# Kernel tuning notes

Hardware: AMD Instinct MI355X
Metric: run time of the kernel (lower is better)

The kernel has to match this reference:

```python
import jax, jax.numpy as jnp
import numpy as np

N, E = 50000, 600000
IN_C, HID, OUT_C = 256, 128, 2
R, B, L = 7, 8, 3
ALPHA = 0.1


def _rgcn(x, src, dst, etype, comp, basis, root, bias):
    # comp: [R,B], basis: [B,d,d] -> per-relation weights W: [R,d,d]
    n, d = x.shape
    W = jnp.einsum('rb,bdf->rdf', comp, basis)
    # combined (dst, relation) segment id for per-relation mean aggregation
    seg = dst * R + etype
    msg = x[src]  # [E,d] gather
    s = jax.ops.segment_sum(msg, seg, num_segments=n * R)  # [N*R,d]
    cnt = jax.ops.segment_sum(jnp.ones((E,), x.dtype), seg, num_segments=n * R)
    agg = (s / jnp.maximum(cnt, 1.0)[:, None]).reshape(n, R, d)  # per-relation mean
    return x @ root + bias + jnp.einsum('nrd,rdf->nf', agg, W)


def setup_inputs() -> dict:
    key = jax.random.key(0)
    ks = jax.random.split(key, 10)
    sc = 0.05
    x = jax.random.normal(ks[0], (N, IN_C), dtype=jnp.float32)
    edge_index = jax.random.randint(ks[1], (2, E), 0, N)
    edge_type = jax.random.randint(ks[2], (E,), 0, R)
    # GPR temp init: alpha*(1-alpha)^k, last entry (1-alpha)^K
    temp = jnp.asarray(ALPHA * (1.0 - ALPHA) ** np.arange(L + 1), dtype=jnp.float32)
    temp = temp.at[-1].set((1.0 - ALPHA) ** L)
    lin1_w = jax.random.normal(ks[3], (IN_C, HID), jnp.float32) * sc
    lin1_b = jnp.zeros((HID,), jnp.float32)
    lin2_w = jax.random.normal(ks[4], (HID, OUT_C), jnp.float32) * sc
    lin2_b = jnp.zeros((OUT_C,), jnp.float32)
    comps = jax.random.normal(ks[5], (L, R, B), jnp.float32) * sc
    bases = jax.random.normal(ks[6], (L, B, HID, HID), jnp.float32) * sc
    roots = jax.random.normal(ks[7], (L, HID, HID), jnp.float32) * sc
    conv_biases = jnp.zeros((L, HID), jnp.float32)
    return dict(x=x, edge_index=edge_index, edge_type=edge_type, temp=temp,
                lin1_w=lin1_w, lin1_b=lin1_b, lin2_w=lin2_w, lin2_b=lin2_b,
                comps=comps, bases=bases, roots=roots, conv_biases=conv_biases)


def reference(x, edge_index, edge_type, temp, lin1_w, lin1_b, lin2_w, lin2_b,
              comps, bases, roots, conv_biases):
    src, dst = edge_index[0], edge_index[1]
    h = x @ lin1_w + lin1_b
    hidden = h * temp[0]
    cur = hidden
    for i in range(L):
        cur = _rgcn(cur, src, dst, edge_type, comps[i], bases[i], roots[i], conv_biases[i])
        if i < L - 1:
            cur = jax.nn.relu(cur)  # dropout p=0.4 is identity in eval mode
        hidden = hidden + temp[i + 1] * cur
    return hidden @ lin2_w + lin2_b
```

## Files before the change

### kernel.cpp

```cpp
#include <hip/hip_runtime.h>
#include <cstdint>


constexpr int N_NODES  = 50000;
constexpr int E_EDGES  = 600000;
constexpr int R_REL    = 7;
constexpr int HID      = 128;
constexpr int IN_C     = 256;
constexpr int L_LAYERS = 3;
constexpr int AGG_COLS = 896;
constexpr int K_CAT    = 1024;
constexpr int NR       = N_NODES * R_REL;
constexpr int SCANR_BLOCKS = (NR + 255) / 256;

#define DEVI __device__ __forceinline__

using short8  = __attribute__((ext_vector_type(8))) short;
using floatx4 = __attribute__((ext_vector_type(4))) float;

DEVI unsigned short f2bf(float f) {
  unsigned u = __float_as_uint(f);
  unsigned r = (u + 0x7FFFu + ((u >> 16) & 1u)) >> 16;
  return (unsigned short)r;
}
DEVI float bf2f(unsigned short h) { return __uint_as_float(((unsigned)h) << 16); }

__global__ __launch_bounds__(256) void cast_w1_kernel(
    const float* __restrict__ w1, unsigned short* __restrict__ w1T)
{
  int t = blockIdx.x * 256 + threadIdx.x;
  if (t >= HID * IN_C) return;
  int m = t >> 8, k = t & 255;
  w1T[m * IN_C + k] = f2bf(w1[k * HID + m]);
}

__global__ __launch_bounds__(256) void build_wcat2(
    const float* __restrict__ comps,
    const float* __restrict__ bases,
    const float* __restrict__ roots,
    unsigned short* __restrict__ wcat2T)
{
  int t = blockIdx.x * 256 + threadIdx.x;
  if (t >= L_LAYERS * 128 * K_CAT) return;
  int l   = t >> 17;
  int rem = t & 131071;
  int f   = rem >> 10;
  int k   = rem & 1023;
  float v;
  if (k < 128) {
    v = roots[((size_t)l * 128 + k) * 128 + f];
  } else {
    int r = (k - 128) >> 7, d = (k - 128) & 127;
    const float* cp = comps + ((size_t)l * R_REL + r) * 8;
    const float* bp = bases + (((size_t)l * 8) * 128 + d) * 128 + f;
    float s = 0.f;
#pragma unroll
    for (int b = 0; b < 8; ++b) s += cp[b] * bp[(size_t)b * 128 * 128];
    v = s;
  }
  wcat2T[t] = f2bf(v);
}

__global__ __launch_bounds__(256) void hist_kernel(
    const int* __restrict__ ei, const int* __restrict__ et,
    int* __restrict__ cntRel, int* __restrict__ erank)
{
  int e = blockIdx.x * 256 + threadIdx.x;
  if (e >= E_EDGES) return;
  int seg = ei[E_EDGES + e] * R_REL + et[e];
  erank[e] = atomicAdd(&cntRel[seg], 1);
}

__global__ __launch_bounds__(256) void scanA_kernel(
    const int* __restrict__ cnt, int* __restrict__ tmpOff,
    int* __restrict__ blockSums)
{
  __shared__ int s[256];
  int i = blockIdx.x * 256 + threadIdx.x;
  int v = (i < NR) ? cnt[i] : 0;
  s[threadIdx.x] = v;
  __syncthreads();
#pragma unroll
  for (int d = 1; d < 256; d <<= 1) {
    int t = (threadIdx.x >= d) ? s[threadIdx.x - d] : 0;
    __syncthreads();
    s[threadIdx.x] += t;
    __syncthreads();
  }
  if (i < NR) tmpOff[i] = s[threadIdx.x] - v;
  if (threadIdx.x == 255) blockSums[blockIdx.x] = s[255];
}

__global__ __launch_bounds__(256) void scanB_kernel(int* __restrict__ bs)
{
  __shared__ int s[256];
  __shared__ int carry;
  if (threadIdx.x == 0) carry = 0;
  __syncthreads();
  for (int base = 0; base < SCANR_BLOCKS; base += 256) {
    int cOld = carry;
    int i = base + threadIdx.x;
    int v = (i < SCANR_BLOCKS) ? bs[i] : 0;
    s[threadIdx.x] = v;
    __syncthreads();
#pragma unroll
    for (int d = 1; d < 256; d <<= 1) {
      int t = (threadIdx.x >= d) ? s[threadIdx.x - d] : 0;
      __syncthreads();
      s[threadIdx.x] += t;
      __syncthreads();
    }
    if (i < SCANR_BLOCKS) bs[i] = s[threadIdx.x] - v + cOld;
    __syncthreads();
    if (threadIdx.x == 0) carry = cOld + s[255];
    __syncthreads();
  }
}

__global__ __launch_bounds__(256) void scanC_kernel(
    const int* __restrict__ tmpOff, const int* __restrict__ blockSums,
    int* __restrict__ drs)
{
  int i = blockIdx.x * 256 + threadIdx.x;
  if (i < NR) drs[i] = tmpOff[i] + blockSums[blockIdx.x];
  if (i == 0) drs[NR] = E_EDGES;
}

__global__ __launch_bounds__(256) void place_kernel(
    const int* __restrict__ ei, const int* __restrict__ et,
    const int* __restrict__ drs, const int* __restrict__ erank,
    unsigned short* __restrict__ esrc)
{
  int e = blockIdx.x * 256 + threadIdx.x;
  if (e >= E_EDGES) return;
  int seg = ei[E_EDGES + e] * R_REL + et[e];
  int pos = drs[seg] + erank[e];
  esrc[pos] = (unsigned short)ei[e];
}

constexpr int AGG_NPF = 16;
__global__ __launch_bounds__(256) void agg_reg_kernel(
    const unsigned short* __restrict__ curA,
    const unsigned short* __restrict__ esrc,
    const int* __restrict__ drs,
    unsigned short* __restrict__ aggB)
{
  const int tid  = threadIdx.x;
  const int lane = tid & 63;
  const int dst  = blockIdx.x * 4 + (tid >> 6);
  if (dst >= N_NODES) return;
  const int segBase = dst * R_REL;

  int bnd = drs[segBase + (lane & 7)];
  const int a0    = __shfl(bnd, 0);
  const int total = __shfl(bnd, 7) - a0;

  int pk = 0;
  if (lane < total) pk = (int)esrc[a0 + lane];

  const unsigned* colp = (const unsigned*)curA + lane;
  unsigned* outp = (unsigned*)(aggB + (size_t)dst * AGG_COLS) + lane;

  int r = 0;
  int segStart = 0;
  int segEnd = __shfl(bnd, 1) - a0;
  float sx = 0.f, sy = 0.f;
  int pos = 0;

#define AGG_FLUSH()                                                        \
  while (r < R_REL && segEnd == pos) {                                     \
    int c = segEnd - segStart;                                             \
    float sc = (c > 0) ? 1.0f / (float)c : 0.f;                            \
    unsigned pck = (unsigned)f2bf(sx * sc) | ((unsigned)f2bf(sy * sc) << 16); \
    outp[r * 64] = pck;                                                    \
    sx = 0.f; sy = 0.f;                                                    \
    segStart = segEnd;                                                     \
    ++r;                                                                   \
    segEnd = (r < R_REL) ? (__shfl(bnd, r + 1) - a0) : 0x7FFFFFFF;         \
  }

  AGG_FLUSH();

  for (int base = 0; base < total; base += AGG_NPF) {
    const int cnt = min(total - base, AGG_NPF);
    unsigned v[AGG_NPF];
#pragma unroll
    for (int e = 0; e < AGG_NPF; ++e) {
      if (e < cnt) {
        int idx = base + e;
        int src = (idx < 64) ? __shfl(pk, idx) : (int)esrc[a0 + idx];
        v[e] = colp[src * 64];
      }
    }
#pragma unroll
    for (int e = 0; e < AGG_NPF; ++e) {
      if (e >= cnt) break;
      unsigned u = v[e];
      sx += __uint_as_float(u << 16);
      sy += __uint_as_float(u & 0xFFFF0000u);
      ++pos;
      AGG_FLUSH();
    }
  }
#undef AGG_FLUSH
}

__global__ __launch_bounds__(256) void gemm_lin1(
    const float* __restrict__ x,
    const unsigned short* __restrict__ BT,
    const float* __restrict__ bias,
    const float* __restrict__ temp,
    unsigned short* __restrict__ b0out)
{
  __shared__ unsigned short Atile[64][136];
  __shared__ unsigned short Btile[128][136];
  const int tid  = threadIdx.x;
  const int row0 = blockIdx.x * 64;
  const int lane = tid & 63;
  const int wid  = tid >> 6;
  const int wrow = (wid & 1) * 32;
  const int wcol = (wid >> 1) * 64;
  const int l15  = lane & 15;
  const int quad = lane >> 4;

  floatx4 acc[2][4] = {};

  for (int k0 = 0; k0 < IN_C; k0 += 128) {
#pragma unroll
    for (int it = 0; it < 4; ++it) {
      int chunk = it * 256 + tid;
      int r = chunk >> 4, cc = (chunk & 15) << 3;
      int grow = row0 + r;
      uint4 va = make_uint4(0u, 0u, 0u, 0u);
      if (grow < N_NODES) {
        const float* xp = x + (size_t)grow * IN_C + k0 + cc;
        float4 f0 = *(const float4*)xp;
        float4 f1 = *(const float4*)(xp + 4);
        va.x = (unsigned)f2bf(f0.x) | ((unsigned)f2bf(f0.y) << 16);
        va.y = (unsigned)f2bf(f0.z) | ((unsigned)f2bf(f0.w) << 16);
        va.z = (unsigned)f2bf(f1.x) | ((unsigned)f2bf(f1.y) << 16);
        va.w = (unsigned)f2bf(f1.z) | ((unsigned)f2bf(f1.w) << 16);
      }
      *(uint4*)(&Atile[r][cc]) = va;
    }
#pragma unroll
    for (int it = 0; it < 8; ++it) {
      int chunk = it * 256 + tid;
      int n = chunk >> 4, cc = (chunk & 15) << 3;
      *(uint4*)(&Btile[n][cc]) =
          *(const uint4*)(BT + (size_t)n * IN_C + k0 + cc);
    }
    __syncthreads();
#pragma unroll
    for (int ks = 0; ks < 4; ++ks) {
      int kc = ks * 32 + quad * 8;
      short8 af[2], bfr[4];
#pragma unroll
      for (int i = 0; i < 2; ++i)
        af[i] = *(const short8*)(&Atile[wrow + i * 16 + l15][kc]);
#pragma unroll
      for (int j = 0; j < 4; ++j)
        bfr[j] = *(const short8*)(&Btile[wcol + j * 16 + l15][kc]);
#pragma unroll
      for (int i = 0; i < 2; ++i)
#pragma unroll
        for (int j = 0; j < 4; ++j)
          acc[i][j] = __builtin_amdgcn_mfma_f32_16x16x32_bf16(
              af[i], bfr[j], acc[i][j], 0, 0, 0);
    }
    __syncthreads();
  }

  float t0 = temp[0];
#pragma unroll
  for (int i = 0; i < 2; ++i) {
    int lrow0 = wrow + i * 16 + quad * 4;
#pragma unroll
    for (int j = 0; j < 4; ++j) {
      int gcol = wcol + j * 16 + l15;
      float bb = bias[gcol];
#pragma unroll
      for (int r = 0; r < 4; ++r)
        Atile[lrow0 + r][gcol] = f2bf(t0 * (acc[i][j][r] + bb));
    }
  }
  __syncthreads();
#pragma unroll
  for (int it = 0; it < 4; ++it) {
    int chunk = it * 256 + tid;
    int r = chunk >> 4, cc = (chunk & 15) << 3;
    int grow = row0 + r;
    if (grow < N_NODES)
      *(uint4*)(b0out + (size_t)grow * HID + cc) = *(const uint4*)(&Atile[r][cc]);
  }
}

__global__ __launch_bounds__(256) void gemm_layer(
    const unsigned short* __restrict__ curA,
    const unsigned short* __restrict__ aggB,
    const unsigned short* __restrict__ BT,
    const float* __restrict__ bias,
    unsigned short* __restrict__ bout,
    int layer)
{
  __shared__ unsigned short Atile[64][136];
  __shared__ unsigned short Btile[128][136];
  const int tid  = threadIdx.x;
  const int row0 = blockIdx.x * 64;
  const int lane = tid & 63;
  const int wid  = tid >> 6;
  const int wrow = (wid & 1) * 32;
  const int wcol = (wid >> 1) * 64;
  const int l15  = lane & 15;
  const int quad = lane >> 4;

  floatx4 acc[2][4] = {};

  for (int p = 0; p < 8; ++p) {
#pragma unroll
    for (int it = 0; it < 8; ++it) {
      int chunk = it * 256 + tid;
      int n = chunk >> 4, cc = (chunk & 15) << 3;
      *(uint4*)(&Btile[n][cc]) =
          *(const uint4*)(BT + (size_t)n * K_CAT + p * 128 + cc);
    }
#pragma unroll
    for (int it = 0; it < 4; ++it) {
      int chunk = it * 256 + tid;
      int r = chunk >> 4, cc = (chunk & 15) << 3;
      int grow = row0 + r;
      uint4 va = make_uint4(0u, 0u, 0u, 0u);
      if (grow < N_NODES) {
        if (p == 0)
          va = *(const uint4*)(curA + (size_t)grow * HID + cc);
        else
          va = *(const uint4*)(aggB + (size_t)grow * AGG_COLS +
                               (p - 1) * 128 + cc);
      }
      *(uint4*)(&Atile[r][cc]) = va;
    }
    __syncthreads();
#pragma unroll
    for (int ks = 0; ks < 4; ++ks) {
      int kc = ks * 32 + quad * 8;
      short8 af[2], bfr[4];
#pragma unroll
      for (int i = 0; i < 2; ++i)
        af[i] = *(const short8*)(&Atile[wrow + i * 16 + l15][kc]);
#pragma unroll
      for (int j = 0; j < 4; ++j)
        bfr[j] = *(const short8*)(&Btile[wcol + j * 16 + l15][kc]);
#pragma unroll
      for (int i = 0; i < 2; ++i)
#pragma unroll
        for (int j = 0; j < 4; ++j)
          acc[i][j] = __builtin_amdgcn_mfma_f32_16x16x32_bf16(
              af[i], bfr[j], acc[i][j], 0, 0, 0);
    }
    __syncthreads();
  }

  const bool isLast = (layer == L_LAYERS - 1);
#pragma unroll
  for (int i = 0; i < 2; ++i) {
    int lrow0 = wrow + i * 16 + quad * 4;
#pragma unroll
    for (int j = 0; j < 4; ++j) {
      int gcol = wcol + j * 16 + l15;
      float bb = bias[gcol];
#pragma unroll
      for (int r = 0; r < 4; ++r) {
        float c = acc[i][j][r] + bb;
        if (!isLast) c = fmaxf(c, 0.f);
        Atile[lrow0 + r][gcol] = f2bf(c);
      }
    }
  }
  __syncthreads();
#pragma unroll
  for (int it = 0; it < 4; ++it) {
    int chunk = it * 256 + tid;
    int r = chunk >> 4, cc = (chunk & 15) << 3;
    int grow = row0 + r;
    if (grow < N_NODES)
      *(uint4*)(bout + (size_t)grow * HID + cc) = *(const uint4*)(&Atile[r][cc]);
  }
}

__global__ __launch_bounds__(256) void final_kernel(
    const unsigned short* __restrict__ b0, const unsigned short* __restrict__ b1,
    const unsigned short* __restrict__ b2v, const unsigned short* __restrict__ b3,
    const float* __restrict__ temp,
    const float* __restrict__ w2, const float* __restrict__ b2bias,
    float* __restrict__ out)
{
  int node = blockIdx.x * 4 + (threadIdx.x >> 6);
  int lane = threadIdx.x & 63;
  if (node >= N_NODES) return;
  float t1 = temp[1], t2 = temp[2], t3 = temp[3];
  size_t base = (size_t)node * 64 + lane;
  unsigned u0 = ((const unsigned*)b0)[base];
  unsigned u1 = ((const unsigned*)b1)[base];
  unsigned u2 = ((const unsigned*)b2v)[base];
  unsigned u3 = ((const unsigned*)b3)[base];
  float hx = bf2f((unsigned short)(u0 & 0xFFFF)) +
             t1 * bf2f((unsigned short)(u1 & 0xFFFF)) +
             t2 * bf2f((unsigned short)(u2 & 0xFFFF)) +
             t3 * bf2f((unsigned short)(u3 & 0xFFFF));
  float hy = bf2f((unsigned short)(u0 >> 16)) +
             t1 * bf2f((unsigned short)(u1 >> 16)) +
             t2 * bf2f((unsigned short)(u2 >> 16)) +
             t3 * bf2f((unsigned short)(u3 >> 16));
  int d0 = lane * 2, d1 = lane * 2 + 1;
  float a0 = hx * w2[d0 * 2 + 0] + hy * w2[d1 * 2 + 0];
  float a1 = hx * w2[d0 * 2 + 1] + hy * w2[d1 * 2 + 1];
#pragma unroll
  for (int off = 32; off > 0; off >>= 1) {
    a0 += __shfl_down(a0, off);
    a1 += __shfl_down(a1, off);
  }
  if (lane == 0) {
    out[node * 2 + 0] = a0 + b2bias[0];
    out[node * 2 + 1] = a1 + b2bias[1];
  }
}

extern "C" void kernel_launch(void* const* d_in, const int* in_sizes, int n_in,
                              void* d_out, int out_size, void* d_ws, size_t ws_size,
                              hipStream_t stream) {
  const float* x     = (const float*)d_in[0];
  const int*   ei    = (const int*)d_in[1];
  const int*   et    = (const int*)d_in[2];
  const float* temp  = (const float*)d_in[3];
  const float* w1    = (const float*)d_in[4];
  const float* b1    = (const float*)d_in[5];
  const float* w2    = (const float*)d_in[6];
  const float* b2    = (const float*)d_in[7];
  const float* comps = (const float*)d_in[8];
  const float* bases = (const float*)d_in[9];
  const float* roots = (const float*)d_in[10];
  const float* cbias = (const float*)d_in[11];

  char* ws = (char*)d_ws;
  size_t off = 0;
  auto take = [&](size_t bytes) {
    char* p = ws + off;
    off = (off + bytes + 255) & ~(size_t)255;
    return p;
  };
  unsigned short* wcat2T = (unsigned short*)take((size_t)L_LAYERS * 128 * K_CAT * 2);
  unsigned short* w1T    = (unsigned short*)take((size_t)HID * IN_C * 2);
  int*   cntRel  = (int*)take((size_t)NR * 4);
  int*   tmpOffR = (int*)take((size_t)NR * 4);
  int*   blockSumsR = (int*)take((size_t)SCANR_BLOCKS * 4);
  int*   drs     = (int*)take((size_t)(NR + 1) * 4);
  int*   erank   = (int*)take((size_t)E_EDGES * 4);
  unsigned short* esrc = (unsigned short*)take((size_t)E_EDGES * 2);
  unsigned short* bl[L_LAYERS + 1];
  for (int i = 0; i <= L_LAYERS; ++i)
    bl[i] = (unsigned short*)take((size_t)N_NODES * HID * 2);
  unsigned short* aggB = (unsigned short*)take((size_t)N_NODES * AGG_COLS * 2);

  hipMemsetAsync(cntRel, 0, (size_t)NR * 4, stream);

  hipLaunchKernelGGL(build_wcat2, dim3((L_LAYERS * 128 * K_CAT + 255) / 256),
                     dim3(256), 0, stream, comps, bases, roots, wcat2T);
  hipLaunchKernelGGL(cast_w1_kernel, dim3((HID * IN_C + 255) / 256), dim3(256),
                     0, stream, w1, w1T);
  hipLaunchKernelGGL(hist_kernel, dim3((E_EDGES + 255) / 256), dim3(256), 0,
                     stream, ei, et, cntRel, erank);
  hipLaunchKernelGGL(scanA_kernel, dim3(SCANR_BLOCKS), dim3(256), 0, stream,
                     cntRel, tmpOffR, blockSumsR);
  hipLaunchKernelGGL(scanB_kernel, dim3(1), dim3(256), 0, stream, blockSumsR);
  hipLaunchKernelGGL(scanC_kernel, dim3(SCANR_BLOCKS), dim3(256), 0, stream,
                     tmpOffR, blockSumsR, drs);
  hipLaunchKernelGGL(place_kernel, dim3((E_EDGES + 255) / 256), dim3(256), 0,
                     stream, ei, et, drs, erank, esrc);

  const int rowBlocks64 = (N_NODES + 63) / 64;
  hipLaunchKernelGGL(gemm_lin1, dim3(rowBlocks64), dim3(256), 0, stream,
                     x, w1T, b1, temp, bl[0]);

  for (int l = 0; l < L_LAYERS; ++l) {
    hipLaunchKernelGGL(agg_reg_kernel, dim3((N_NODES + 3) / 4), dim3(256),
                       0, stream, bl[l], esrc, drs, aggB);
    hipLaunchKernelGGL(gemm_layer, dim3(rowBlocks64), dim3(256), 0, stream,
                       bl[l], aggB, wcat2T + (size_t)l * 128 * K_CAT,
                       cbias + (size_t)l * HID, bl[l + 1], l);
  }

  hipLaunchKernelGGL(final_kernel, dim3((N_NODES + 3) / 4), dim3(256), 0, stream,
                     bl[0], bl[1], bl[2], bl[3], temp, w2, b2, (float*)d_out);
}
```

Measured before the change: 496.5 us.

## Load GEMM A fragments directly from global and widen row tile to 128

The layer GEMM now reads its A operand (current features and aggregated neighbours) straight from global memory into MFMA registers, no longer staging it in shared memory, and each block covers 128 rows instead of 64 with a 4x4 accumulator grid per wave. This halves how often the shared B tile is reloaded per row and removes A's LDS traffic, at the cost of more registers and uncoalesced 16-byte row-strided global loads. The two weight-preparation kernels are also merged into one launch to save a kernel launch.

```diff
diff --git a/kernel.cpp b/kernel.cpp
--- a/kernel.cpp
+++ b/kernel.cpp
@@ -12,6 +12,7 @@
 constexpr int K_CAT    = 1024;
 constexpr int NR       = N_NODES * R_REL;
 constexpr int SCANR_BLOCKS = (NR + 255) / 256;
+constexpr int WCAT_ELEMS = L_LAYERS * 128 * K_CAT;
 
 #define DEVI __device__ __forceinline__
 
@@ -25,40 +26,40 @@
 }
 DEVI float bf2f(unsigned short h) { return __uint_as_float(((unsigned)h) << 16); }
 
-__global__ __launch_bounds__(256) void cast_w1_kernel(
-    const float* __restrict__ w1, unsigned short* __restrict__ w1T)
-{
-  int t = blockIdx.x * 256 + threadIdx.x;
-  if (t >= HID * IN_C) return;
-  int m = t >> 8, k = t & 255;
-  w1T[m * IN_C + k] = f2bf(w1[k * HID + m]);
-}
-
-__global__ __launch_bounds__(256) void build_wcat2(
+__global__ __launch_bounds__(256) void prep_weights(
+    const float* __restrict__ w1,
     const float* __restrict__ comps,
     const float* __restrict__ bases,
     const float* __restrict__ roots,
+    unsigned short* __restrict__ w1T,
     unsigned short* __restrict__ wcat2T)
 {
   int t = blockIdx.x * 256 + threadIdx.x;
-  if (t >= L_LAYERS * 128 * K_CAT) return;
-  int l   = t >> 17;
-  int rem = t & 131071;
-  int f   = rem >> 10;
-  int k   = rem & 1023;
-  float v;
-  if (k < 128) {
-    v = roots[((size_t)l * 128 + k) * 128 + f];
+  if (t < WCAT_ELEMS) {
+    int l   = t >> 17;
+    int rem = t & 131071;
+    int f   = rem >> 10;
+    int k   = rem & 1023;
+    float v;
+    if (k < 128) {
+      v = roots[((size_t)l * 128 + k) * 128 + f];
+    } else {
+      int r = (k - 128) >> 7, d = (k - 128) & 127;
+      const float* cp = comps + ((size_t)l * R_REL + r) * 8;
+      const float* bp = bases + (((size_t)l * 8) * 128 + d) * 128 + f;
+      float s = 0.f;
+#pragma unroll
+      for (int b = 0; b < 8; ++b) s += cp[b] * bp[(size_t)b * 128 * 128];
+      v = s;
+    }
+    wcat2T[t] = f2bf(v);
   } else {
-    int r = (k - 128) >> 7, d = (k - 128) & 127;
-    const float* cp = comps + ((size_t)l * R_REL + r) * 8;
-    const float* bp = bases + (((size_t)l * 8) * 128 + d) * 128 + f;
-    float s = 0.f;
-#pragma unroll
-    for (int b = 0; b < 8; ++b) s += cp[b] * bp[(size_t)b * 128 * 128];
-    v = s;
-  }
-  wcat2T[t] = f2bf(v);
+    int u = t - WCAT_ELEMS;
+    if (u < HID * IN_C) {
+      int m = u >> 8, k = u & 255;
+      w1T[m * IN_C + k] = f2bf(w1[k * HID + m]);
+    }
+  }
 }
 
 __global__ __launch_bounds__(256) void hist_kernel(
@@ -303,18 +304,17 @@
     unsigned short* __restrict__ bout,
     int layer)
 {
-  __shared__ unsigned short Atile[64][136];
   __shared__ unsigned short Btile[128][136];
   const int tid  = threadIdx.x;
-  const int row0 = blockIdx.x * 64;
+  const int row0 = blockIdx.x * 128;
   const int lane = tid & 63;
   const int wid  = tid >> 6;
-  const int wrow = (wid & 1) * 32;
+  const int wrow = (wid & 1) * 64;
   const int wcol = (wid >> 1) * 64;
   const int l15  = lane & 15;
   const int quad = lane >> 4;
 
-  floatx4 acc[2][4] = {};
+  floatx4 acc[4][4] = {};
 
   for (int p = 0; p < 8; ++p) {
 #pragma unroll
@@ -324,34 +324,28 @@
       *(uint4*)(&Btile[n][cc]) =
           *(const uint4*)(BT + (size_t)n * K_CAT + p * 128 + cc);
     }
-#pragma unroll
-    for (int it = 0; it < 4; ++it) {
-      int chunk = it * 256 + tid;
-      int r = chunk >> 4, cc = (chunk & 15) << 3;
-      int grow = row0 + r;
-      uint4 va = make_uint4(0u, 0u, 0u, 0u);
-      if (grow < N_NODES) {
-        if (p == 0)
-          va = *(const uint4*)(curA + (size_t)grow * HID + cc);
-        else
-          va = *(const uint4*)(aggB + (size_t)grow * AGG_COLS +
-                               (p - 1) * 128 + cc);
-      }
-      *(uint4*)(&Atile[r][cc]) = va;
-    }
     __syncthreads();
 #pragma unroll
     for (int ks = 0; ks < 4; ++ks) {
       int kc = ks * 32 + quad * 8;
-      short8 af[2], bfr[4];
-#pragma unroll
-      for (int i = 0; i < 2; ++i)
-        af[i] = *(const short8*)(&Atile[wrow + i * 16 + l15][kc]);
+      short8 af[4], bfr[4];
+#pragma unroll
+      for (int i = 0; i < 4; ++i) {
+        int grow = row0 + wrow + i * 16 + l15;
+        short8 v = {};
+        if (grow < N_NODES) {
+          const unsigned short* ap = (p == 0)
+              ? curA + (size_t)grow * HID + kc
+              : aggB + (size_t)grow * AGG_COLS + (p - 1) * 128 + kc;
+          v = *(const short8*)ap;
+        }
+        af[i] = v;
+      }
 #pragma unroll
       for (int j = 0; j < 4; ++j)
         bfr[j] = *(const short8*)(&Btile[wcol + j * 16 + l15][kc]);
 #pragma unroll
-      for (int i = 0; i < 2; ++i)
+      for (int i = 0; i < 4; ++i)
 #pragma unroll
         for (int j = 0; j < 4; ++j)
           acc[i][j] = __builtin_amdgcn_mfma_f32_16x16x32_bf16(
@@ -362,7 +356,7 @@
 
   const bool isLast = (layer == L_LAYERS - 1);
 #pragma unroll
-  for (int i = 0; i < 2; ++i) {
+  for (int i = 0; i < 4; ++i) {
     int lrow0 = wrow + i * 16 + quad * 4;
 #pragma unroll
     for (int j = 0; j < 4; ++j) {
@@ -372,18 +366,18 @@
       for (int r = 0; r < 4; ++r) {
         float c = acc[i][j][r] + bb;
         if (!isLast) c = fmaxf(c, 0.f);
-        Atile[lrow0 + r][gcol] = f2bf(c);
+        Btile[lrow0 + r][gcol] = f2bf(c);
       }
     }
   }
   __syncthreads();
 #pragma unroll
-  for (int it = 0; it < 4; ++it) {
+  for (int it = 0; it < 8; ++it) {
     int chunk = it * 256 + tid;
     int r = chunk >> 4, cc = (chunk & 15) << 3;
     int grow = row0 + r;
     if (grow < N_NODES)
-      *(uint4*)(bout + (size_t)grow * HID + cc) = *(const uint4*)(&Atile[r][cc]);
+      *(uint4*)(bout + (size_t)grow * HID + cc) = *(const uint4*)(&Btile[r][cc]);
   }
 }
 
@@ -448,7 +442,7 @@
     off = (off + bytes + 255) & ~(size_t)255;
     return p;
   };
-  unsigned short* wcat2T = (unsigned short*)take((size_t)L_LAYERS * 128 * K_CAT * 2);
+  unsigned short* wcat2T = (unsigned short*)take((size_t)WCAT_ELEMS * 2);
   unsigned short* w1T    = (unsigned short*)take((size_t)HID * IN_C * 2);
   int*   cntRel  = (int*)take((size_t)NR * 4);
   int*   tmpOffR = (int*)take((size_t)NR * 4);
@@ -463,10 +457,9 @@
 
   hipMemsetAsync(cntRel, 0, (size_t)NR * 4, stream);
 
-  hipLaunchKernelGGL(build_wcat2, dim3((L_LAYERS * 128 * K_CAT + 255) / 256),
-                     dim3(256), 0, stream, comps, bases, roots, wcat2T);
-  hipLaunchKernelGGL(cast_w1_kernel, dim3((HID * IN_C + 255) / 256), dim3(256),
-                     0, stream, w1, w1T);
+  hipLaunchKernelGGL(prep_weights,
+                     dim3((WCAT_ELEMS + HID * IN_C + 255) / 256), dim3(256),
+                     0, stream, w1, comps, bases, roots, w1T, wcat2T);
   hipLaunchKernelGGL(hist_kernel, dim3((E_EDGES + 255) / 256), dim3(256), 0,
                      stream, ei, et, cntRel, erank);
   hipLaunchKernelGGL(scanA_kernel, dim3(SCANR_BLOCKS), dim3(256), 0, stream,
@@ -477,14 +470,15 @@
   hipLaunchKernelGGL(place_kernel, dim3((E_EDGES + 255) / 256), dim3(256), 0,
                      stream, ei, et, drs, erank, esrc);
 
-  const int rowBlocks64 = (N_NODES + 63) / 64;
+  const int rowBlocks64  = (N_NODES + 63) / 64;
+  const int rowBlocks128 = (N_NODES + 127) / 128;
   hipLaunchKernelGGL(gemm_lin1, dim3(rowBlocks64), dim3(256), 0, stream,
                      x, w1T, b1, temp, bl[0]);
 
   for (int l = 0; l < L_LAYERS; ++l) {
     hipLaunchKernelGGL(agg_reg_kernel, dim3((N_NODES + 3) / 4), dim3(256),
                        0, stream, bl[l], esrc, drs, aggB);
-    hipLaunchKernelGGL(gemm_layer, dim3(rowBlocks64), dim3(256), 0, stream,
+    hipLaunchKernelGGL(gemm_layer, dim3(rowBlocks128), dim3(256), 0, stream,
                        bl[l], aggB, wcat2T + (size_t)l * 128 * K_CAT,
                        cbias + (size_t)l * HID, bl[l + 1], l);
   }
```

After: 478.6 us. 1.04x faster.
